# Optimization experiments

Hardware: AMD Instinct MI355X
Metric: run time of the kernel (lower is better)

The kernel has to match this reference:

```python
import jax, jax.numpy as jnp
import numpy as np

N = 100000   # nodes
E = 1600000  # edges (avg degree 16)
IN = 64
HID = 16     # hardcoded in ChebNet.conv1
OUT = 40
K = 3


def setup_inputs() -> dict:
    key = jax.random.key(0)
    k0, k1, k2, k3 = jax.random.split(key, 4)
    x = jax.random.normal(k0, (N, IN), jnp.float32)
    edge_index = jax.random.randint(k1, (2, E), 0, N, jnp.int32)
    # Glorot-style init for the K per-order linear maps of each ChebConv
    s1 = float(np.sqrt(2.0 / (IN + HID)))
    W1 = jax.random.normal(k2, (K, IN, HID), jnp.float32) * s1
    b1 = jnp.zeros((HID,), jnp.float32)
    s2 = float(np.sqrt(2.0 / (HID + OUT)))
    W2 = jax.random.normal(k3, (K, HID, OUT), jnp.float32) * s2
    b2 = jnp.zeros((OUT,), jnp.float32)
    return {"x": x, "edge_index": edge_index, "W1": W1, "b1": b1, "W2": W2, "b2": b2}


def cheb_conv(x, edge_index, W, b):
    """PyG ChebConv with normalization='sym', lambda_max=2.
    Scaled Laplacian: L_hat = 2L/lambda_max - I = -D^{-1/2} A D^{-1/2} (diag 0).
    out = sum_k T_k(L_hat) x @ W[k] + b, T0=x, T1=L_hat x, Tk=2 L_hat T_{k-1}-T_{k-2}.
    """
    row, col = edge_index[0], edge_index[1]
    ones = jnp.ones((edge_index.shape[1],), x.dtype)
    deg = jax.ops.segment_sum(ones, row, num_segments=N)
    dis = jnp.where(deg > 0, jax.lax.rsqrt(jnp.maximum(deg, 1.0)), 0.0)
    norm = -(dis[row] * dis[col])  # [E]

    def Lhat(z):  # sparse scatter-gather: gather src rows, scale, scatter-add to dst
        return jax.ops.segment_sum(norm[:, None] * z[row], col, num_segments=N)

    Tx0 = x
    out = Tx0 @ W[0]
    Tx1 = Lhat(x)
    if W.shape[0] > 1:
        out = out + Tx1 @ W[1]
    for k in range(2, W.shape[0]):
        Tx2 = 2.0 * Lhat(Tx1) - Tx0
        out = out + Tx2 @ W[k]
        Tx0, Tx1 = Tx1, Tx2
    return out + b


def reference(x, edge_index, W1, b1, W2, b2):
    h = jax.nn.relu(cheb_conv(x, edge_index, W1, b1))
    h = cheb_conv(h, edge_index, W2, b2)
    return jax.nn.log_softmax(h, axis=1)
```

## Files before the change

### kernel.cpp

```cpp
#include <hip/hip_runtime.h>
#include <hip/hip_bf16.h>


typedef unsigned short ushort_t;

constexpr int N_   = 100000;
constexpr int E_   = 1600000;
constexpr int IN_  = 64;
constexpr int HID_ = 16;
constexpr int OUT_ = 40;
constexpr int CAP_ = 48;
constexpr int P_   = 8;
constexpr int S_   = 64;
constexpr int NPP_ = N_ / P_;
constexpr int EPS_ = E_ / S_;

__device__ __forceinline__ float bf2f(ushort_t u) {
    return __uint_as_float((unsigned)u << 16);
}
__device__ __forceinline__ ushort_t f2bf(float x) {
    unsigned u = __float_as_uint(x);
    return (ushort_t)((u + 0x7FFFu + ((u >> 16) & 1u)) >> 16);
}

__global__ void deg_part(const int* __restrict__ row, int* __restrict__ partial) {
    __shared__ int lds[NPP_];
    int p = blockIdx.x >> 6, s = blockIdx.x & 63;
    for (int i = threadIdx.x; i < NPP_; i += 256) lds[i] = 0;
    __syncthreads();
    int lo = p * NPP_;
    int e0 = s * EPS_;
    for (int i = threadIdx.x; i < EPS_; i += 256) {
        int r = row[e0 + i];
        unsigned d = (unsigned)(r - lo);
        if (d < (unsigned)NPP_) atomicAdd(&lds[d], 1);
    }
    __syncthreads();
    int* dst = partial + (size_t)blockIdx.x * NPP_;
    for (int i = threadIdx.x; i < NPP_; i += 256) dst[i] = lds[i];
}

__global__ void deg_reduce(const int* __restrict__ partial, float* __restrict__ dis) {
    int n = blockIdx.x * 256 + threadIdx.x;
    if (n >= N_) return;
    int p = n / NPP_, i = n - p * NPP_;
    const int* base = partial + (size_t)(p * S_) * NPP_ + i;
    int d = 0;
#pragma unroll 8
    for (int s = 0; s < S_; ++s) d += base[(size_t)s * NPP_];
    dis[n] = (d > 0) ? rsqrtf((float)d) : 0.0f;
}

__global__ void bucket_proj(const int* __restrict__ row, const int* __restrict__ col,
                            const float* __restrict__ x, const float* __restrict__ W,
                            const float* __restrict__ dis,
                            int* __restrict__ cnt, int* __restrict__ bucket,
                            float* __restrict__ P0f, float* __restrict__ P2f,
                            ushort_t* __restrict__ A1, ushort_t* __restrict__ A2) {
    __shared__ float w[3 * IN_ * HID_];
    int role = blockIdx.x & 1, idx = blockIdx.x >> 1;
    if (role == 0) {
        int e = idx * 256 + threadIdx.x;
        int r = row[e], c = col[e];
        int p = atomicAdd(&cnt[c], 1);
        if (p < CAP_) bucket[c * CAP_ + p] = r;
    } else {
        for (int i = threadIdx.x; i < 3 * IN_ * HID_; i += 256) w[i] = W[i];
        __syncthreads();
        int t = idx * 256 + threadIdx.x;
        int n = t >> 4, j = t & 15;
        const float* xr = x + (size_t)n * IN_;
        float a0 = 0.f, a1 = 0.f, a2 = 0.f;
#pragma unroll
        for (int i = 0; i < IN_; ++i) {
            float xv = xr[i];
            a0 += xv * w[i * 16 + j];
            a1 += xv * w[1024 + i * 16 + j];
            a2 += xv * w[2048 + i * 16 + j];
        }
        float dn = dis[n];
        P0f[t] = a0;
        P2f[t] = a2;
        A1[t] = f2bf(dn * a1);
        A2[t] = f2bf(dn * a2);
    }
}

__global__ void g32b(const ushort_t* __restrict__ A1, const ushort_t* __restrict__ A2,
                     const int* __restrict__ cnt, const int* __restrict__ bucket,
                     const float* __restrict__ dis,
                     float* __restrict__ LP1f, ushort_t* __restrict__ B2) {
    int wib = threadIdx.x >> 6, lane = threadIdx.x & 63;
    int n0 = (blockIdx.x * 4 + wib) * 4;
    int eg = lane >> 3, sub = lane & 7;
    const ushort_t* Z = (sub < 4) ? A1 : A2;
    int fq = sub & 3;
    int m[4];
#pragma unroll
    for (int k = 0; k < 4; ++k) m[k] = min(cnt[n0 + k], CAP_);
    float ax[4] = {0,0,0,0}, ay[4] = {0,0,0,0}, az[4] = {0,0,0,0}, aw[4] = {0,0,0,0};
#pragma unroll
    for (int k = 0; k < 4; ++k) {
        int n = n0 + k;
        for (int base = 0; base < m[k]; base += 8) {
            int e = base + eg;
            if (e < m[k]) {
                int r = bucket[n * CAP_ + e];
                ushort4 zv = *(const ushort4*)&Z[(size_t)r * 16 + fq * 4];
                ax[k] += bf2f(zv.x); ay[k] += bf2f(zv.y);
                az[k] += bf2f(zv.z); aw[k] += bf2f(zv.w);
            }
        }
    }
#pragma unroll
    for (int off = 8; off < 64; off <<= 1) {
#pragma unroll
        for (int k = 0; k < 4; ++k) {
            ax[k] += __shfl_xor(ax[k], off, 64); ay[k] += __shfl_xor(ay[k], off, 64);
            az[k] += __shfl_xor(az[k], off, 64); aw[k] += __shfl_xor(aw[k], off, 64);
        }
    }
    if (lane < 8) {
#pragma unroll
        for (int k = 0; k < 4; ++k) {
            int n = n0 + k;
            float dn = dis[n];
            if (lane < 4) {
                float4 v = {-dn * ax[k], -dn * ay[k], -dn * az[k], -dn * aw[k]};
                *(float4*)&LP1f[(size_t)n * 16 + fq * 4] = v;
            } else {
                float s = -(dn * dn);
                ushort4 v = {f2bf(s * ax[k]), f2bf(s * ay[k]),
                             f2bf(s * az[k]), f2bf(s * aw[k])};
                *(ushort4*)&B2[(size_t)n * 16 + fq * 4] = v;
            }
        }
    }
}

__device__ __forceinline__ void g16core4(const ushort_t* __restrict__ Z,
                                         const int* __restrict__ cnt,
                                         const int* __restrict__ bucket,
                                         int n0, int lane, float4 acc[4]) {
    int eg = lane >> 2, fq = lane & 3;
    int m[4];
#pragma unroll
    for (int k = 0; k < 4; ++k) m[k] = min(cnt[n0 + k], CAP_);
    float ax[4] = {0,0,0,0}, ay[4] = {0,0,0,0}, az[4] = {0,0,0,0}, aw[4] = {0,0,0,0};
#pragma unroll
    for (int k = 0; k < 4; ++k) {
        int n = n0 + k;
        for (int base = 0; base < m[k]; base += 16) {
            int e = base + eg;
            if (e < m[k]) {
                int r = bucket[n * CAP_ + e];
                ushort4 zv = *(const ushort4*)&Z[(size_t)r * 16 + fq * 4];
                ax[k] += bf2f(zv.x); ay[k] += bf2f(zv.y);
                az[k] += bf2f(zv.z); aw[k] += bf2f(zv.w);
            }
        }
    }
#pragma unroll
    for (int off = 4; off < 64; off <<= 1) {
#pragma unroll
        for (int k = 0; k < 4; ++k) {
            ax[k] += __shfl_xor(ax[k], off, 64); ay[k] += __shfl_xor(ay[k], off, 64);
            az[k] += __shfl_xor(az[k], off, 64); aw[k] += __shfl_xor(aw[k], off, 64);
        }
    }
#pragma unroll
    for (int k = 0; k < 4; ++k) {
        float4 r4 = {ax[k], ay[k], az[k], aw[k]};
        acc[k] = r4;
    }
}

__global__ void g16_combine(const ushort_t* __restrict__ B2, const int* __restrict__ cnt,
                            const int* __restrict__ bucket, const float* __restrict__ dis,
                            const float* __restrict__ LP1f, const float* __restrict__ P2f,
                            const float* __restrict__ b1,
                            float* p0h , ushort_t* __restrict__ Hs) {
    int wib = threadIdx.x >> 6, lane = threadIdx.x & 63;
    int n0 = (blockIdx.x * 4 + wib) * 4;
    float4 acc[4];
    g16core4(B2, cnt, bucket, n0, lane, acc);
    if (lane < 4) {
#pragma unroll
        for (int k = 0; k < 4; ++k) {
            int n = n0 + k;
            float dn = dis[n];
            float4 p0 = *(const float4*)&p0h[(size_t)n * 16 + lane * 4];
            float4 lp = *(const float4*)&LP1f[(size_t)n * 16 + lane * 4];
            float4 p2 = *(const float4*)&P2f[(size_t)n * 16 + lane * 4];
            float4 bb = *(const float4*)&b1[lane * 4];
            float4 hv;
            hv.x = fmaxf(p0.x + lp.x - 2.f * dn * acc[k].x - p2.x + bb.x, 0.f);
            hv.y = fmaxf(p0.y + lp.y - 2.f * dn * acc[k].y - p2.y + bb.y, 0.f);
            hv.z = fmaxf(p0.z + lp.z - 2.f * dn * acc[k].z - p2.z + bb.z, 0.f);
            hv.w = fmaxf(p0.w + lp.w - 2.f * dn * acc[k].w - p2.w + bb.w, 0.f);
            *(float4*)&p0h[(size_t)n * 16 + lane * 4] = hv;
            ushort4 hs = {f2bf(dn * hv.x), f2bf(dn * hv.y),
                          f2bf(dn * hv.z), f2bf(dn * hv.w)};
            *(ushort4*)&Hs[(size_t)n * 16 + lane * 4] = hs;
        }
    }
}

__global__ void g16_t1(const ushort_t* __restrict__ Hs, const int* __restrict__ cnt,
                       const int* __restrict__ bucket, const float* __restrict__ dis,
                       float* __restrict__ T1f, ushort_t* __restrict__ Ts) {
    int wib = threadIdx.x >> 6, lane = threadIdx.x & 63;
    int n0 = (blockIdx.x * 4 + wib) * 4;
    float4 acc[4];
    g16core4(Hs, cnt, bucket, n0, lane, acc);
    if (lane < 4) {
#pragma unroll
        for (int k = 0; k < 4; ++k) {
            int n = n0 + k;
            float dn = dis[n];
            float4 t1 = {-dn * acc[k].x, -dn * acc[k].y, -dn * acc[k].z, -dn * acc[k].w};
            *(float4*)&T1f[(size_t)n * 16 + lane * 4] = t1;
            ushort4 ts = {f2bf(dn * t1.x), f2bf(dn * t1.y),
                          f2bf(dn * t1.z), f2bf(dn * t1.w)};
            *(ushort4*)&Ts[(size_t)n * 16 + lane * 4] = ts;
        }
    }
}

__global__ void g16_mm2_lsm(const ushort_t* __restrict__ Ts, const int* __restrict__ cnt,
                            const int* __restrict__ bucket, const float* __restrict__ dis,
                            const float* __restrict__ Hf, const float* __restrict__ T1f,
                            const float* __restrict__ W2, const float* __restrict__ b2,
                            float* __restrict__ out) {
    __shared__ float w[3 * HID_ * OUT_];
    __shared__ float t2s[4][4][16];
    for (int i = threadIdx.x; i < 3 * HID_ * OUT_; i += blockDim.x) w[i] = W2[i];
    int wib = threadIdx.x >> 6, lane = threadIdx.x & 63;
    int n0 = (blockIdx.x * 4 + wib) * 4;
    float4 acc[4];
    g16core4(Ts, cnt, bucket, n0, lane, acc);
    if (lane < 4) {
#pragma unroll
        for (int k = 0; k < 4; ++k) {
            int n = n0 + k;
            float dn = dis[n];
            float4 h4 = *(const float4*)&Hf[(size_t)n * 16 + lane * 4];
            float4 t2;
            t2.x = -2.f * dn * acc[k].x - h4.x;
            t2.y = -2.f * dn * acc[k].y - h4.y;
            t2.z = -2.f * dn * acc[k].z - h4.z;
            t2.w = -2.f * dn * acc[k].w - h4.w;
            *(float4*)&t2s[wib][k][lane * 4] = t2;
        }
    }
    __syncthreads();
#pragma unroll
    for (int k = 0; k < 4; ++k) {
        int n = n0 + k;
        float a2 = -3.0e38f;
        if (lane < OUT_) {
            a2 = b2[lane];
            const float* hr  = Hf + (size_t)n * 16;
            const float* t1r = T1f + (size_t)n * 16;
#pragma unroll
            for (int j = 0; j < HID_; ++j) {
                a2 += hr[j] * w[j * OUT_ + lane]
                    + t1r[j] * w[640 + j * OUT_ + lane]
                    + t2s[wib][k][j] * w[1280 + j * OUT_ + lane];
            }
        }
        float mx = a2;
#pragma unroll
        for (int off = 32; off > 0; off >>= 1) mx = fmaxf(mx, __shfl_xor(mx, off, 64));
        float ev = (lane < OUT_) ? __expf(a2 - mx) : 0.0f;
        float s = ev;
#pragma unroll
        for (int off = 32; off > 0; off >>= 1) s += __shfl_xor(s, off, 64);
        float ls = logf(s);
        if (lane < OUT_) out[(size_t)n * OUT_ + lane] = a2 - mx - ls;
    }
}


extern "C" void kernel_launch(void* const* d_in, const int* in_sizes, int n_in,
                              void* d_out, int out_size, void* d_ws, size_t ws_size,
                              hipStream_t stream) {
    const float* x  = (const float*)d_in[0];
    const int*   ei = (const int*)d_in[1];
    const float* W1 = (const float*)d_in[2];
    const float* b1 = (const float*)d_in[3];
    const float* W2 = (const float*)d_in[4];
    const float* b2 = (const float*)d_in[5];
    float* out = (float*)d_out;

    const int* row = ei;
    const int* col = ei + E_;

    char* wp = (char*)d_ws;
    int*      cnt    = (int*)wp;      wp += 401408;
    float*    dis    = (float*)wp;    wp += 401408;
    int*      bucket = (int*)wp;      wp += (size_t)N_ * CAP_ * 4;
    ushort_t* A1     = (ushort_t*)wp; wp += 3211264;
    ushort_t* A2     = (ushort_t*)wp; wp += 3211264;
    ushort_t* B2     = (ushort_t*)wp; wp += 3211264;
    float*    P0f    = (float*)wp;    wp += 6422528;
    float*    P2f    = (float*)wp;    wp += 6422528;
    float*    LP1f   = (float*)wp;    wp += 6422528;

    int*      partial = (int*)A1;
    float*    Hf  = P0f;
    ushort_t* Hs  = A1;
    float*    T1f = LP1f;
    ushort_t* Ts  = A2;

    hipMemsetAsync(cnt, 0, N_ * sizeof(int), stream);

    deg_part<<<P_ * S_, 256, 0, stream>>>(row, partial);
    deg_reduce<<<(N_ + 255) / 256, 256, 0, stream>>>(partial, dis);

    bucket_proj<<<12500, 256, 0, stream>>>(row, col, x, W1, dis, cnt, bucket,
                                           P0f, P2f, A1, A2);

    g32b<<<N_ / 16, 256, 0, stream>>>(A1, A2, cnt, bucket, dis, LP1f, B2);
    g16_combine<<<N_ / 16, 256, 0, stream>>>(B2, cnt, bucket, dis, LP1f, P2f, b1,
                                             P0f , Hs);
    g16_t1<<<N_ / 16, 256, 0, stream>>>(Hs, cnt, bucket, dis, T1f, Ts);
    g16_mm2_lsm<<<N_ / 16, 256, 0, stream>>>(Ts, cnt, bucket, dis, Hf, T1f, W2, b2, out);
}
```

Before: 386.7 us.

## Replace global-atomic bucket fill with LDS histogram prefix placement

Builds the per-destination edge buckets deterministically. A partitioned LDS histogram of in-degrees is reduced into per-slice prefix offsets, and edges are then placed using LDS atomics instead of global atomicAdd on a count array. This removes contended global atomics and the memset of the count array. In exchange it adds a histogram kernel and a 64-slice prefix array, and partial counts are narrowed to 16-bit. The bucket order within each node becomes slice-ordered.

After: 380.2 us. No clear change (-1.7%).

```diff
diff --git a/kernel.cpp b/kernel.cpp
--- a/kernel.cpp
+++ b/kernel.cpp
@@ -2,72 +2,118 @@
 #include <hip/hip_bf16.h>
 
 
-typedef unsigned short ushort_t;
-
-constexpr int N_   = 100000;
-constexpr int E_   = 1600000;
-constexpr int IN_  = 64;
-constexpr int HID_ = 16;
-constexpr int OUT_ = 40;
-constexpr int CAP_ = 48;
-constexpr int P_   = 8;
-constexpr int S_   = 64;
-constexpr int NPP_ = N_ / P_;
-constexpr int EPS_ = E_ / S_;
-
-__device__ __forceinline__ float bf2f(ushort_t u) {
+typedef unsigned short u16;
+
+constexpr int N_    = 100000;
+constexpr int E_    = 1600000;
+constexpr int IN_   = 64;
+constexpr int HID_  = 16;
+constexpr int OUT_  = 40;
+constexpr int CAP_  = 48;
+constexpr int S_    = 64;
+constexpr int EPS_  = E_ / S_;
+constexpr int P8_   = 8;
+constexpr int NPP8_ = N_ / P8_;
+constexpr int P4_   = 4;
+constexpr int NPP4_ = N_ / P4_;
+constexpr int NPAD_ = 100352;
+
+__device__ __forceinline__ float bf2f(u16 u) {
     return __uint_as_float((unsigned)u << 16);
 }
-__device__ __forceinline__ ushort_t f2bf(float x) {
+__device__ __forceinline__ u16 f2bf(float x) {
     unsigned u = __float_as_uint(x);
-    return (ushort_t)((u + 0x7FFFu + ((u >> 16) & 1u)) >> 16);
-}
-
-__global__ void deg_part(const int* __restrict__ row, int* __restrict__ partial) {
-    __shared__ int lds[NPP_];
+    return (u16)((u + 0x7FFFu + ((u >> 16) & 1u)) >> 16);
+}
+
+__global__ void deg_part(const int* __restrict__ row, u16* __restrict__ partial) {
+    __shared__ int lds[NPP8_];
     int p = blockIdx.x >> 6, s = blockIdx.x & 63;
-    for (int i = threadIdx.x; i < NPP_; i += 256) lds[i] = 0;
-    __syncthreads();
-    int lo = p * NPP_;
-    int e0 = s * EPS_;
+    for (int i = threadIdx.x; i < NPP8_; i += 256) lds[i] = 0;
+    __syncthreads();
+    int lo = p * NPP8_, e0 = s * EPS_;
     for (int i = threadIdx.x; i < EPS_; i += 256) {
         int r = row[e0 + i];
         unsigned d = (unsigned)(r - lo);
-        if (d < (unsigned)NPP_) atomicAdd(&lds[d], 1);
-    }
-    __syncthreads();
-    int* dst = partial + (size_t)blockIdx.x * NPP_;
-    for (int i = threadIdx.x; i < NPP_; i += 256) dst[i] = lds[i];
-}
-
-__global__ void deg_reduce(const int* __restrict__ partial, float* __restrict__ dis) {
-    int n = blockIdx.x * 256 + threadIdx.x;
+        if (d < (unsigned)NPP8_) atomicAdd(&lds[d], 1);
+    }
+    __syncthreads();
+    u16* dst = partial + (size_t)blockIdx.x * NPP8_;
+    for (int i = threadIdx.x; i < NPP8_; i += 256) dst[i] = (u16)lds[i];
+}
+
+__global__ void __launch_bounds__(1024)
+hist_in(const int* __restrict__ col, u16* __restrict__ partial) {
+    __shared__ int lds[NPP4_];
+    int p = blockIdx.x >> 6, s = blockIdx.x & 63;
+    for (int i = threadIdx.x; i < NPP4_; i += 1024) lds[i] = 0;
+    __syncthreads();
+    int lo = p * NPP4_, e0 = s * EPS_;
+    for (int i = threadIdx.x; i < EPS_; i += 1024) {
+        int c = col[e0 + i];
+        unsigned d = (unsigned)(c - lo);
+        if (d < (unsigned)NPP4_) atomicAdd(&lds[d], 1);
+    }
+    __syncthreads();
+    u16* dst = partial + (size_t)blockIdx.x * NPP4_;
+    for (int i = threadIdx.x; i < NPP4_; i += 1024) dst[i] = (u16)lds[i];
+}
+
+__global__ void __launch_bounds__(1024)
+reduce_all(const u16* __restrict__ partial_row, const u16* __restrict__ partial_in,
+           float* __restrict__ dis, u16* __restrict__ pre, int* __restrict__ indeg) {
+    int n = blockIdx.x * 1024 + threadIdx.x;
     if (n >= N_) return;
-    int p = n / NPP_, i = n - p * NPP_;
-    const int* base = partial + (size_t)(p * S_) * NPP_ + i;
-    int d = 0;
+    {
+        int p = n / NPP8_, i = n - p * NPP8_;
+        const u16* base = partial_row + (size_t)(p * S_) * NPP8_ + i;
+        int d = 0;
 #pragma unroll 8
-    for (int s = 0; s < S_; ++s) d += base[(size_t)s * NPP_];
-    dis[n] = (d > 0) ? rsqrtf((float)d) : 0.0f;
-}
-
-__global__ void bucket_proj(const int* __restrict__ row, const int* __restrict__ col,
-                            const float* __restrict__ x, const float* __restrict__ W,
-                            const float* __restrict__ dis,
-                            int* __restrict__ cnt, int* __restrict__ bucket,
-                            float* __restrict__ P0f, float* __restrict__ P2f,
-                            ushort_t* __restrict__ A1, ushort_t* __restrict__ A2) {
+        for (int s = 0; s < S_; ++s) d += base[(size_t)s * NPP8_];
+        dis[n] = (d > 0) ? rsqrtf((float)d) : 0.0f;
+    }
+    {
+        int p = n / NPP4_, i = n - p * NPP4_;
+        const u16* base = partial_in + (size_t)(p * S_) * NPP4_ + i;
+        int run = 0;
+#pragma unroll 8
+        for (int s = 0; s < S_; ++s) {
+            pre[(size_t)s * NPAD_ + n] = (u16)run;
+            run += base[(size_t)s * NPP4_];
+        }
+        indeg[n] = run;
+    }
+}
+
+__global__ void __launch_bounds__(1024)
+place_proj(const int* __restrict__ row, const int* __restrict__ col,
+           const float* __restrict__ x, const float* __restrict__ W,
+           const float* __restrict__ dis, const u16* __restrict__ pre,
+           int* __restrict__ bucket,
+           float* __restrict__ P0f, float* __restrict__ P2f,
+           u16* __restrict__ A1, u16* __restrict__ A2) {
+    __shared__ int pos[NPP4_];
     __shared__ float w[3 * IN_ * HID_];
-    int role = blockIdx.x & 1, idx = blockIdx.x >> 1;
-    if (role == 0) {
-        int e = idx * 256 + threadIdx.x;
-        int r = row[e], c = col[e];
-        int p = atomicAdd(&cnt[c], 1);
-        if (p < CAP_) bucket[c * CAP_ + p] = r;
+    if (blockIdx.x < 256) {
+        int p = blockIdx.x >> 6, s = blockIdx.x & 63;
+        int lo = p * NPP4_, e0 = s * EPS_;
+        const u16* psrc = pre + (size_t)s * NPAD_ + lo;
+        for (int i = threadIdx.x; i < NPP4_; i += 1024) pos[i] = psrc[i];
+        __syncthreads();
+        for (int i = threadIdx.x; i < EPS_; i += 1024) {
+            int c = col[e0 + i];
+            unsigned d = (unsigned)(c - lo);
+            if (d < (unsigned)NPP4_) {
+                int r = row[e0 + i];
+                int q = atomicAdd(&pos[d], 1);
+                if (q < CAP_) bucket[(size_t)c * CAP_ + q] = r;
+            }
+        }
     } else {
-        for (int i = threadIdx.x; i < 3 * IN_ * HID_; i += 256) w[i] = W[i];
+        for (int i = threadIdx.x; i < 3 * IN_ * HID_; i += 1024) w[i] = W[i];
         __syncthreads();
-        int t = idx * 256 + threadIdx.x;
+        int t = (blockIdx.x - 256) * 1024 + threadIdx.x;
+        if (t >= N_ * HID_) return;
         int n = t >> 4, j = t & 15;
         const float* xr = x + (size_t)n * IN_;
         float a0 = 0.f, a1 = 0.f, a2 = 0.f;
@@ -86,18 +132,18 @@
     }
 }
 
-__global__ void g32b(const ushort_t* __restrict__ A1, const ushort_t* __restrict__ A2,
-                     const int* __restrict__ cnt, const int* __restrict__ bucket,
+__global__ void g32b(const u16* __restrict__ A1, const u16* __restrict__ A2,
+                     const int* __restrict__ indeg, const int* __restrict__ bucket,
                      const float* __restrict__ dis,
-                     float* __restrict__ LP1f, ushort_t* __restrict__ B2) {
+                     float* __restrict__ LP1f, u16* __restrict__ B2) {
     int wib = threadIdx.x >> 6, lane = threadIdx.x & 63;
     int n0 = (blockIdx.x * 4 + wib) * 4;
     int eg = lane >> 3, sub = lane & 7;
-    const ushort_t* Z = (sub < 4) ? A1 : A2;
+    const u16* Z = (sub < 4) ? A1 : A2;
     int fq = sub & 3;
     int m[4];
 #pragma unroll
-    for (int k = 0; k < 4; ++k) m[k] = min(cnt[n0 + k], CAP_);
+    for (int k = 0; k < 4; ++k) m[k] = min(indeg[n0 + k], CAP_);
     float ax[4] = {0,0,0,0}, ay[4] = {0,0,0,0}, az[4] = {0,0,0,0}, aw[4] = {0,0,0,0};
 #pragma unroll
     for (int k = 0; k < 4; ++k) {
@@ -138,14 +184,14 @@
     }
 }
 
-__device__ __forceinline__ void g16core4(const ushort_t* __restrict__ Z,
-                                         const int* __restrict__ cnt,
+__device__ __forceinline__ void g16core4(const u16* __restrict__ Z,
+                                         const int* __restrict__ indeg,
                                          const int* __restrict__ bucket,
                                          int n0, int lane, float4 acc[4]) {
     int eg = lane >> 2, fq = lane & 3;
     int m[4];
 #pragma unroll
-    for (int k = 0; k < 4; ++k) m[k] = min(cnt[n0 + k], CAP_);
+    for (int k = 0; k < 4; ++k) m[k] = min(indeg[n0 + k], CAP_);
     float ax[4] = {0,0,0,0}, ay[4] = {0,0,0,0}, az[4] = {0,0,0,0}, aw[4] = {0,0,0,0};
 #pragma unroll
     for (int k = 0; k < 4; ++k) {
@@ -175,15 +221,15 @@
     }
 }
 
-__global__ void g16_combine(const ushort_t* __restrict__ B2, const int* __restrict__ cnt,
+__global__ void g16_combine(const u16* __restrict__ B2, const int* __restrict__ indeg,
                             const int* __restrict__ bucket, const float* __restrict__ dis,
                             const float* __restrict__ LP1f, const float* __restrict__ P2f,
                             const float* __restrict__ b1,
-                            float* p0h , ushort_t* __restrict__ Hs) {
+                            float* p0h , u16* __restrict__ Hs) {
     int wib = threadIdx.x >> 6, lane = threadIdx.x & 63;
     int n0 = (blockIdx.x * 4 + wib) * 4;
     float4 acc[4];
-    g16core4(B2, cnt, bucket, n0, lane, acc);
+    g16core4(B2, indeg, bucket, n0, lane, acc);
     if (lane < 4) {
 #pragma unroll
         for (int k = 0; k < 4; ++k) {
@@ -206,13 +252,13 @@
     }
 }
 
-__global__ void g16_t1(const ushort_t* __restrict__ Hs, const int* __restrict__ cnt,
+__global__ void g16_t1(const u16* __restrict__ Hs, const int* __restrict__ indeg,
                        const int* __restrict__ bucket, const float* __restrict__ dis,
-                       float* __restrict__ T1f, ushort_t* __restrict__ Ts) {
+                       float* __restrict__ T1f, u16* __restrict__ Ts) {
     int wib = threadIdx.x >> 6, lane = threadIdx.x & 63;
     int n0 = (blockIdx.x * 4 + wib) * 4;
     float4 acc[4];
-    g16core4(Hs, cnt, bucket, n0, lane, acc);
+    g16core4(Hs, indeg, bucket, n0, lane, acc);
     if (lane < 4) {
 #pragma unroll
         for (int k = 0; k < 4; ++k) {
@@ -227,7 +273,7 @@
     }
 }
 
-__global__ void g16_mm2_lsm(const ushort_t* __restrict__ Ts, const int* __restrict__ cnt,
+__global__ void g16_mm2_lsm(const u16* __restrict__ Ts, const int* __restrict__ indeg,
                             const int* __restrict__ bucket, const float* __restrict__ dis,
                             const float* __restrict__ Hf, const float* __restrict__ T1f,
                             const float* __restrict__ W2, const float* __restrict__ b2,
@@ -238,7 +284,7 @@
     int wib = threadIdx.x >> 6, lane = threadIdx.x & 63;
     int n0 = (blockIdx.x * 4 + wib) * 4;
     float4 acc[4];
-    g16core4(Ts, cnt, bucket, n0, lane, acc);
+    g16core4(Ts, indeg, bucket, n0, lane, acc);
     if (lane < 4) {
 #pragma unroll
         for (int k = 0; k < 4; ++k) {
@@ -297,33 +343,37 @@
     const int* col = ei + E_;
 
     char* wp = (char*)d_ws;
-    int*      cnt    = (int*)wp;      wp += 401408;
-    float*    dis    = (float*)wp;    wp += 401408;
-    int*      bucket = (int*)wp;      wp += (size_t)N_ * CAP_ * 4;
-    ushort_t* A1     = (ushort_t*)wp; wp += 3211264;
-    ushort_t* A2     = (ushort_t*)wp; wp += 3211264;
-    ushort_t* B2     = (ushort_t*)wp; wp += 3211264;
-    float*    P0f    = (float*)wp;    wp += 6422528;
-    float*    P2f    = (float*)wp;    wp += 6422528;
-    float*    LP1f   = (float*)wp;    wp += 6422528;
-
-    int*      partial = (int*)A1;
-    float*    Hf  = P0f;
-    ushort_t* Hs  = A1;
-    float*    T1f = LP1f;
-    ushort_t* Ts  = A2;
-
-    hipMemsetAsync(cnt, 0, N_ * sizeof(int), stream);
-
-    deg_part<<<P_ * S_, 256, 0, stream>>>(row, partial);
-    deg_reduce<<<(N_ + 255) / 256, 256, 0, stream>>>(partial, dis);
-
-    bucket_proj<<<12500, 256, 0, stream>>>(row, col, x, W1, dis, cnt, bucket,
-                                           P0f, P2f, A1, A2);
-
-    g32b<<<N_ / 16, 256, 0, stream>>>(A1, A2, cnt, bucket, dis, LP1f, B2);
-    g16_combine<<<N_ / 16, 256, 0, stream>>>(B2, cnt, bucket, dis, LP1f, P2f, b1,
+    float* dis    = (float*)wp;  wp += 401408;
+    int*   indeg  = (int*)wp;    wp += 401408;
+    int*   bucket = (int*)wp;    wp += (size_t)N_ * CAP_ * 4;
+    u16*   pre    = (u16*)wp;    wp += (size_t)S_ * NPAD_ * 2;
+    char*  region = wp;
+    u16* partial_row = (u16*)region;
+    u16* partial_in  = (u16*)(region + 12800000);
+    wp = region;
+    u16*   A1   = (u16*)wp;   wp += 3211264;
+    u16*   A2   = (u16*)wp;   wp += 3211264;
+    u16*   B2   = (u16*)wp;   wp += 3211264;
+    float* P0f  = (float*)wp; wp += 6422528;
+    float* P2f  = (float*)wp; wp += 6422528;
+    float* LP1f = (float*)wp; wp += 6422528;
+
+    float* Hf  = P0f;
+    u16*   Hs  = A1;
+    float* T1f = LP1f;
+    u16*   Ts  = A2;
+
+    deg_part<<<P8_ * S_, 256, 0, stream>>>(row, partial_row);
+    hist_in<<<P4_ * S_, 1024, 0, stream>>>(col, partial_in);
+    reduce_all<<<NPAD_ / 1024, 1024, 0, stream>>>(partial_row, partial_in,
+                                                  dis, pre, indeg);
+    place_proj<<<256 + 1563, 1024, 0, stream>>>(row, col, x, W1, dis, pre,
+                                                bucket, P0f, P2f, A1, A2);
+
+    g32b<<<N_ / 16, 256, 0, stream>>>(A1, A2, indeg, bucket, dis, LP1f, B2);
+    g16_combine<<<N_ / 16, 256, 0, stream>>>(B2, indeg, bucket, dis, LP1f, P2f, b1,
                                              P0f , Hs);
-    g16_t1<<<N_ / 16, 256, 0, stream>>>(Hs, cnt, bucket, dis, T1f, Ts);
-    g16_mm2_lsm<<<N_ / 16, 256, 0, stream>>>(Ts, cnt, bucket, dis, Hf, T1f, W2, b2, out);
-}
+    g16_t1<<<N_ / 16, 256, 0, stream>>>(Hs, indeg, bucket, dis, T1f, Ts);
+    g16_mm2_lsm<<<N_ / 16, 256, 0, stream>>>(Ts, indeg, bucket, dis, Hf, T1f,
+                                             W2, b2, out);
+}
```
